# Optimization experiments

Measured on AMD Instinct MI355X. Metric: run time of the kernel, lower is better.

## Reference

```python
import jax, jax.numpy as jnp
import numpy as np

PI = float(np.pi)
N_BINS_POT = 140
TIMESTEP = 0.02
ATOMS = ["N", "CA", "C", "cent"]
ANGLES = [("N", "CA", "C", 0), ("CA", "C", "N", 1), ("C", "N", "CA", 2), ("N", "CA", "cent", 0), ("C", "CA", "cent", 0)]
DIHEDRALS = [("C", "N", "CA", "C", 3), ("N", "CA", "C", "N", 1), ("CA", "C", "N", "CA", 2), ("C", "N", "CA", "cent", 3), ("cent", "CA", "C", "N", 1)]

_gap_ang = (PI - PI / 3) / N_BINS_POT
ANGLE_CENTRES = np.array([PI / 3 + i * _gap_ang + 0.5 * _gap_ang for i in range(N_BINS_POT)][1:-1], dtype=np.float32)  # 138
_gap_dih = 2 * PI / N_BINS_POT
DIH_CENTRES = np.array([-PI + i * _gap_dih - 0.5 * _gap_dih for i in range(N_BINS_POT + 2)][1:-1], dtype=np.float32)  # 140


def safe_norm(v, axis=-1, keepdims=False):
    sq = jnp.sum(v * v, axis=axis, keepdims=keepdims)
    return jnp.where(sq > 0, jnp.sqrt(jnp.where(sq > 0, sq, 1.0)), 0.0)


def normalize(v):
    # torch.nn.functional.normalize with eps=1e-12
    return v / jnp.maximum(safe_norm(v, keepdims=True), 1e-12)


def _gather_force(pots, inds):
    # pots: [n, n_bins]; inds: [b, n] -> 0.5 * (pots[r, i] - pots[r, i+2])
    r = jnp.arange(pots.shape[0])[None, :]
    return 0.5 * (pots[r, inds] - pots[r, inds + 2])


def _accelerations(coords, masses, pair_centres, pair_pots, angle_pots, dih_pots):
    b, n_atoms, _ = coords.shape
    n_res = n_atoms // 4
    # ---- all-pairs distance forces (bin by argmin against per-pair centres, gather) ----
    diffs = coords[:, None, :, :] - coords[:, :, None, :]  # [b, i, j, 3] = c[j] - c[i]
    dists = safe_norm(diffs)  # [b, i, j]
    df = dists.reshape(b, n_atoms * n_atoms)
    inds = jnp.argmin(jnp.abs(pair_centres[None] - df[:, :, None]), axis=2)  # [b, n^2]
    pair_forces = _gather_force(pair_pots, inds).reshape(b, n_atoms, n_atoms)
    norm_diffs = diffs / jnp.maximum(dists, 0.01)[..., None]
    accs = jnp.sum(pair_forces[..., None] * norm_diffs, axis=1) / masses[..., None]
    # ---- bond-angle forces ----
    ac = coords.reshape(b, n_res, 4, 3)
    aa = jnp.zeros_like(ac)
    ang_centres = jnp.asarray(ANGLE_CENTRES)
    for ai, (a1, a2, a3, across) in enumerate(ANGLES):
        i1, i2, i3 = ATOMS.index(a1), ATOMS.index(a2), ATOMS.index(a3)
        if across == 0:
            ba = ac[:, :, i1] - ac[:, :, i2]; bc = ac[:, :, i3] - ac[:, :, i2]; pots = angle_pots[ai]
        elif across == 1:
            ba = ac[:, :-1, i1] - ac[:, :-1, i2]; bc = ac[:, 1:, i3] - ac[:, :-1, i2]; pots = angle_pots[ai][:-1]
        else:
            ba = ac[:, :-1, i1] - ac[:, 1:, i2]; bc = ac[:, 1:, i3] - ac[:, 1:, i2]; pots = angle_pots[ai][1:]
        ban = safe_norm(ba); bcn = safe_norm(bc)
        angs = jnp.arccos(jnp.sum(ba * bc, axis=2) / (ban * bcn))
        ainds = jnp.argmin(jnp.abs(ang_centres[None, None] - angs[:, :, None]), axis=2)
        f = _gather_force(pots, ainds)[..., None]
        cr = jnp.cross(ba, bc)
        fa = f * normalize(jnp.cross(ba, cr)) / ban[..., None]
        fc = f * normalize(jnp.cross(-bc, cr)) / bcn[..., None]
        fb = -fa - fc
        if across == 0:
            aa = aa.at[:, :, i1].add(fa).at[:, :, i2].add(fb).at[:, :, i3].add(fc)
        elif across == 1:
            aa = aa.at[:, :-1, i1].add(fa).at[:, :-1, i2].add(fb).at[:, 1:, i3].add(fc)
        else:
            aa = aa.at[:, :-1, i1].add(fa).at[:, 1:, i2].add(fb).at[:, 1:, i3].add(fc)
    # ---- dihedral forces ----
    dih_centres = jnp.asarray(DIH_CENTRES)
    for di, (a1, a2, a3, a4, across) in enumerate(DIHEDRALS):
        i1, i2, i3, i4 = ATOMS.index(a1), ATOMS.index(a2), ATOMS.index(a3), ATOMS.index(a4)
        if across == 1:
            ab = ac[:, :-1, i2] - ac[:, :-1, i1]; bc = ac[:, :-1, i3] - ac[:, :-1, i2]; cd = ac[:, 1:, i4] - ac[:, :-1, i3]
            pots = dih_pots[di][:-1]
        elif across == 2:
            ab = ac[:, :-1, i2] - ac[:, :-1, i1]; bc = ac[:, 1:, i3] - ac[:, :-1, i2]; cd = ac[:, 1:, i4] - ac[:, 1:, i3]
            pots = dih_pots[di][1:]
        else:  # across == 3
            ab = ac[:, 1:, i2] - ac[:, :-1, i1]; bc = ac[:, 1:, i3] - ac[:, 1:, i2]; cd = ac[:, 1:, i4] - ac[:, 1:, i3]
            pots = dih_pots[di][1:]
        c1 = jnp.cross(ab, bc); c2 = jnp.cross(bc, cd)
        bcn = safe_norm(bc, keepdims=True)
        dihs = jnp.arctan2(jnp.sum(jnp.cross(c1, c2) * bc / bcn, axis=2), jnp.sum(c1 * c2, axis=2))
        dinds = jnp.argmin(jnp.abs(dih_centres[None, None] - dihs[:, :, None]), axis=2)
        f = _gather_force(pots, dinds)[..., None]
        fa = f * normalize(-c1) / safe_norm(ab, keepdims=True)
        fd = f * normalize(c2) / safe_norm(cd, keepdims=True)
        bsq = jnp.squeeze(bcn, -1) ** 2
        t1 = (jnp.sum(ab * bc, axis=2) / bsq)[..., None]
        t2 = (jnp.sum(cd * bc, axis=2) / bsq)[..., None]
        fb = -fa - t1 * fa + t2 * fd  # torque-balancing middle-atom forces
        fc = -fa - fb - fd
        if across == 1:
            aa = aa.at[:, :-1, i1].add(fa).at[:, :-1, i2].add(fb).at[:, :-1, i3].add(fc).at[:, 1:, i4].add(fd)
        elif across == 2:
            aa = aa.at[:, :-1, i1].add(fa).at[:, :-1, i2].add(fb).at[:, 1:, i3].add(fc).at[:, 1:, i4].add(fd)
        else:
            aa = aa.at[:, :-1, i1].add(fa).at[:, 1:, i2].add(fb).at[:, 1:, i3].add(fc).at[:, 1:, i4].add(fd)
    return accs + aa.reshape(b, n_atoms, 3) / masses[..., None]


def _simulate(coords, vels, masses, ff_distances, ff_angles, ff_dihedrals,
              dist_bin_centres, inters_flat, inters_ang, inters_dih, n_steps):
    pair_centres = dist_bin_centres[inters_flat]  # [n^2, 138]
    pair_pots = ff_distances[inters_flat]         # [n^2, 140]
    angle_pots = ff_angles[:, inters_ang]         # [5, n_res, 140]
    dih_pots = ff_dihedrals[:, inters_dih]        # [5, n_res, 142]

    def step(carry, _):
        c, v, a_last = carry
        c = c + v * TIMESTEP + 0.5 * a_last * TIMESTEP * TIMESTEP
        a = _accelerations(c, masses, pair_centres, pair_pots, angle_pots, dih_pots)
        v = v + 0.5 * (a_last + a) * TIMESTEP
        return (c, v, a), None

    (coords, vels, _), _ = jax.lax.scan(step, (coords, vels, jnp.zeros_like(coords)), None, length=n_steps)
    return coords


def setup_inputs() -> dict:
    key = jax.random.key(0)
    ks = jax.random.split(key, 10)
    b, n_res = 1, 100
    n_atoms = n_res * 4
    n2 = n_atoms * n_atoms
    n_dist_types = 4000
    coords = jax.random.normal(ks[0], (b, n_atoms, 3), jnp.float32) * 10.0
    vels = jax.random.normal(ks[1], (b, n_atoms, 3), jnp.float32) * 0.1  # start_temperature = 0.1
    masses = jax.random.uniform(ks[2], (b, n_atoms), jnp.float32, 0.5, 1.5)
    native_coords = jax.random.normal(ks[3], (b, n_atoms, 3), jnp.float32) * 10.0
    ff_distances = jax.random.normal(ks[4], (n_dist_types, 140), jnp.float32) * 0.1
    ff_angles = jax.random.normal(ks[5], (5, 20, 140), jnp.float32) * 0.1
    ff_dihedrals = jax.random.normal(ks[6], (5, 20, 142), jnp.float32) * 0.1
    centres = jnp.linspace(1.0, 15.9, 138, dtype=jnp.float32)
    dist_bin_centres = jnp.tile(centres[None, :], (n_dist_types, 1))
    inters_flat = jax.random.randint(ks[7], (n2,), 0, n_dist_types)
    inters_ang = jax.random.randint(ks[8], (n_res,), 0, 20)
    inters_dih = jax.random.randint(ks[9], (n_res,), 0, 20)
    return {"coords": coords, "vels": vels, "masses": masses, "native_coords": native_coords,
            "ff_distances": ff_distances, "ff_angles": ff_angles, "ff_dihedrals": ff_dihedrals,
            "dist_bin_centres": dist_bin_centres, "inters_flat": inters_flat,
            "inters_ang": inters_ang, "inters_dih": inters_dih, "n_steps": 3}


def reference(coords, vels, masses, native_coords, ff_distances, ff_angles, ff_dihedrals,
              dist_bin_centres, inters_flat, inters_ang, inters_dih, n_steps):
    # native_coords is only used for RMSD reporting in the original; it does not affect the dynamics.
    return _simulate(coords, vels, masses, ff_distances, ff_angles, ff_dihedrals,
                     dist_bin_centres, inters_flat, inters_ang, inters_dih, n_steps)
```

## Files before the change

### kernel.cpp

```cpp
#include <hip/hip_runtime.h>
#include <math.h>

#define N_ATOMS 400
#define N_RES   100
#define DT      0.02f
#define PI_D    3.14159265358979323846
#define NBLK    100
#define NTHR    256

struct V3 { float x, y, z; };
__device__ __forceinline__ V3 v3(float x, float y, float z) { V3 r{x,y,z}; return r; }
__device__ __forceinline__ V3 sub(V3 a, V3 b) { return v3(a.x-b.x, a.y-b.y, a.z-b.z); }
__device__ __forceinline__ V3 neg(V3 a) { return v3(-a.x, -a.y, -a.z); }
__device__ __forceinline__ V3 scale(V3 a, float s) { return v3(a.x*s, a.y*s, a.z*s); }
__device__ __forceinline__ float dot3(V3 a, V3 b) { return a.x*b.x + a.y*b.y + a.z*b.z; }
__device__ __forceinline__ V3 cross3(V3 a, V3 b) {
    return v3(a.y*b.z - a.z*b.y, a.z*b.x - a.x*b.z, a.x*b.y - a.y*b.x);
}
__device__ __forceinline__ float vnorm(V3 a) {
    float s = dot3(a, a);
    return s > 0.0f ? sqrtf(s) : 0.0f;
}
__device__ __forceinline__ V3 normalize3(V3 a) {
    float n = fmaxf(vnorm(a), 1e-12f);
    return scale(a, 1.0f/n);
}

__device__ __forceinline__ int clampi(int i, int lo, int hi) {
    return i < lo ? lo : (i > hi ? hi : i);
}
__device__ __forceinline__ int bin_dist(float d) {
    const float INV = (float)(137.0/14.9);
    return clampi((int)floorf((d - 1.0f)*INV + 0.5f), 0, 137);
}
__device__ __forceinline__ int bin_ang(float a) {
    const float C0  = (float)(PI_D/3.0 + 1.5*((PI_D - PI_D/3.0)/140.0));
    const float INV = (float)(140.0/(PI_D - PI_D/3.0));
    return clampi((int)floorf((a - C0)*INV + 0.5f), 0, 137);
}
__device__ __forceinline__ int bin_dih(float a) {
    const float C0  = (float)(-PI_D + 0.5*(2.0*PI_D/140.0));
    const float INV = (float)(140.0/(2.0*PI_D));
    return clampi((int)floorf((a - C0)*INV + 0.5f), 0, 139);
}

__constant__ int ANG_I[5][3]   = {{0,1,2},{1,2,0},{2,0,1},{0,1,3},{2,1,3}};
__constant__ int ANG_ACROSS[5] = {0,1,2,0,0};
__constant__ int DIH_I[5][4]   = {{2,0,1,2},{0,1,2,0},{1,2,0,1},{2,0,1,3},{3,1,2,0}};
__constant__ int DIH_ACROSS[5] = {3,1,2,3,1};

__device__ __forceinline__ V3 ldpos(const float* c, int res, int atom) {
    int k = (res*4 + atom)*3;
    return v3(c[k], c[k+1], c[k+2]);
}

__device__ __forceinline__ void addOwn(float* sF, int b, int res, int atom, V3 f) {
    if (res == b) {
        atomicAdd(&sF[atom*3+0], f.x);
        atomicAdd(&sF[atom*3+1], f.y);
        atomicAdd(&sF[atom*3+2], f.z);
    }
}

__device__ __forceinline__ void bonded_own(int u, int b, const float* sc,
                              const float* __restrict__ ffa, const float* __restrict__ ffdih,
                              const int* __restrict__ ia, const int* __restrict__ idh,
                              float* sF) {
    int e = u % 10, which = u / 10;
    int r = b - which;
    if (e < 5) {
        int across = ANG_ACROSS[e];
        bool valid = which ? (b >= 1 && across != 0)
                           : (across == 0 || b <= N_RES-2);
        if (!valid) return;
        int i1 = ANG_I[e][0], i2 = ANG_I[e][1], i3 = ANG_I[e][2];
        int o2 = (across == 2) ? 1 : 0;
        int o3 = (across != 0) ? 1 : 0;
        V3 p1 = ldpos(sc, r,     i1);
        V3 p2 = ldpos(sc, r+o2,  i2);
        V3 p3 = ldpos(sc, r+o3,  i3);
        V3 ba = sub(p1, p2);
        V3 bc = sub(p3, p2);
        float ban = vnorm(ba), bcn = vnorm(bc);
        float ca = dot3(ba, bc) / (ban*bcn);
        ca = fminf(1.0f, fmaxf(-1.0f, ca));
        float ang = acosf(ca);
        int ind = bin_ang(ang);
        int potr = (across == 2) ? r+1 : r;
        const float* row = ffa + (e*20 + ia[potr])*140;
        float f = 0.5f*(row[ind] - row[ind+2]);
        V3 cr = cross3(ba, bc);
        V3 fa = scale(normalize3(cross3(ba, cr)), f/ban);
        V3 fc = scale(normalize3(neg(cross3(bc, cr))), f/bcn);
        V3 fb = neg(v3(fa.x+fc.x, fa.y+fc.y, fa.z+fc.z));
        addOwn(sF, b, r,     i1, fa);
        addOwn(sF, b, r+o2,  i2, fb);
        addOwn(sF, b, r+o3,  i3, fc);
    } else {
        int di = e - 5;
        bool valid = which ? (b >= 1) : (b <= N_RES-2);
        if (!valid) return;
        int across = DIH_ACROSS[di];
        int i1 = DIH_I[di][0], i2 = DIH_I[di][1], i3 = DIH_I[di][2], i4 = DIH_I[di][3];
        int o2 = (across == 3) ? 1 : 0;
        int o3 = (across >= 2) ? 1 : 0;
        int o4 = 1;
        V3 p1 = ldpos(sc, r,     i1);
        V3 p2 = ldpos(sc, r+o2,  i2);
        V3 p3 = ldpos(sc, r+o3,  i3);
        V3 p4 = ldpos(sc, r+o4,  i4);
        V3 ab = sub(p2, p1);
        V3 bc = sub(p3, p2);
        V3 cd = sub(p4, p3);
        V3 c1 = cross3(ab, bc);
        V3 c2 = cross3(bc, cd);
        float bcn = vnorm(bc);
        V3 cc = cross3(c1, c2);
        float y = dot3(cc, bc) / bcn;
        float x = dot3(c1, c2);
        float dih = atan2f(y, x);
        int ind = bin_dih(dih);
        int potr = (across == 1) ? r : r+1;
        const float* row = ffdih + (di*20 + idh[potr])*142;
        float f = 0.5f*(row[ind] - row[ind+2]);
        V3 fa = scale(normalize3(neg(c1)), f / vnorm(ab));
        V3 fd = scale(normalize3(c2),      f / vnorm(cd));
        float bsq = bcn*bcn;
        float t1 = dot3(ab, bc)/bsq;
        float t2 = dot3(cd, bc)/bsq;
        V3 fb = v3(-fa.x - t1*fa.x + t2*fd.x,
                   -fa.y - t1*fa.y + t2*fd.y,
                   -fa.z - t1*fa.z + t2*fd.z);
        V3 fc = v3(-fa.x - fb.x - fd.x,
                   -fa.y - fb.y - fd.y,
                   -fa.z - fb.z - fd.z);
        addOwn(sF, b, r,     i1, fa);
        addOwn(sF, b, r+o2,  i2, fb);
        addOwn(sF, b, r+o3,  i3, fc);
        addOwn(sF, b, r+o4,  i4, fd);
    }
}

__device__ __forceinline__ void grid_barrier(int* bar) {
    __syncthreads();
    if (threadIdx.x == 0) {
        __hip_atomic_fetch_add(bar, 1, __ATOMIC_RELEASE, __HIP_MEMORY_SCOPE_AGENT);
        int iters = 0;
        while (__hip_atomic_load(bar, __ATOMIC_RELAXED, __HIP_MEMORY_SCOPE_AGENT) < NBLK) {
            __builtin_amdgcn_s_sleep(1);
            if (++iters > (1 << 24)) break;
        }
        (void)__hip_atomic_load(bar, __ATOMIC_ACQUIRE, __HIP_MEMORY_SCOPE_AGENT);
    }
    __syncthreads();
}

__global__ void init_kernel(const float* __restrict__ cin, const float* __restrict__ vin,
                            float* __restrict__ c, int* __restrict__ bar) {
    int t = blockIdx.x*blockDim.x + threadIdx.x;
    if (t < N_ATOMS*3) c[t] = cin[t] + vin[t]*DT;
    if (t < 4) bar[t] = 0;
}

__global__ void __launch_bounds__(NTHR)
sim_kernel(const float* __restrict__ vin, const float* __restrict__ masses,
           const float* __restrict__ ffd, const float* __restrict__ ffa,
           const float* __restrict__ ffdih, const int* __restrict__ iflat,
           const int* __restrict__ ia, const int* __restrict__ idh,
           float* __restrict__ out, float* __restrict__ c, int* __restrict__ bar)
{
    __shared__ float sc[N_ATOMS*3];
    __shared__ float sF[12];
    const int tid  = threadIdx.x;
    const int b    = blockIdx.x;
    const int lane = tid & 63;
    const int wave = tid >> 6;
    const int j    = b*4 + wave;

    float vv = 0.0f, aa = 0.0f;
    if (tid < 12) vv = vin[b*12 + tid];

    for (int s = 0; s < 2; ++s) {
        for (int t = tid; t < N_ATOMS*3; t += NTHR)
            sc[t] = __hip_atomic_load(&c[t], __ATOMIC_RELAXED, __HIP_MEMORY_SCOPE_AGENT);
        if (tid < 12) sF[tid] = 0.0f;
        __syncthreads();

        if (tid < 20) bonded_own(tid, b, sc, ffa, ffdih, ia, idh, sF);

        float cx = sc[3*j], cy = sc[3*j+1], cz = sc[3*j+2];
        float fx = 0.0f, fy = 0.0f, fz = 0.0f;
        #pragma unroll
        for (int k = 0; k < 7; ++k) {
            int i = lane + 64*k;
            if (k < 6 || i < N_ATOMS) {
                float dx = cx - sc[3*i];
                float dy = cy - sc[3*i+1];
                float dz = cz - sc[3*i+2];
                float d2 = dx*dx + dy*dy + dz*dz;
                float d  = d2 > 0.0f ? sqrtf(d2) : 0.0f;
                int ind  = bin_dist(d);
                int type = iflat[i*N_ATOMS + j];
                const float* row = ffd + type*140;
                float f = 0.5f*(row[ind] - row[ind+2]);
                float w = f / fmaxf(d, 0.01f);
                fx += w*dx; fy += w*dy; fz += w*dz;
            }
        }
        #pragma unroll
        for (int off = 32; off > 0; off >>= 1) {
            fx += __shfl_down(fx, off);
            fy += __shfl_down(fy, off);
            fz += __shfl_down(fz, off);
        }
        if (lane == 0) {
            atomicAdd(&sF[wave*3+0], fx);
            atomicAdd(&sF[wave*3+1], fy);
            atomicAdd(&sF[wave*3+2], fz);
        }
        __syncthreads();

        if (tid < 12) {
            int t = b*12 + tid;
            float a = sF[tid] / masses[b*4 + tid/3];
            vv += 0.5f*(aa + a)*DT;
            aa = a;
            float cc = sc[t] + vv*DT + 0.5f*a*DT*DT;
            if (s == 0)
                __hip_atomic_store(&c[t], cc, __ATOMIC_RELAXED, __HIP_MEMORY_SCOPE_AGENT);
            else
                out[t] = cc;
        }
        if (s == 0) grid_barrier(bar);
    }
}

extern "C" void kernel_launch(void* const* d_in, const int* in_sizes, int n_in,
                              void* d_out, int out_size, void* d_ws, size_t ws_size,
                              hipStream_t stream) {
    const float* coords = (const float*)d_in[0];
    const float* vels   = (const float*)d_in[1];
    const float* masses = (const float*)d_in[2];
    const float* ffd    = (const float*)d_in[4];
    const float* ffa    = (const float*)d_in[5];
    const float* ffdih  = (const float*)d_in[6];
    const int* iflat    = (const int*)d_in[8];
    const int* ia       = (const int*)d_in[9];
    const int* idh      = (const int*)d_in[10];
    float* out = (float*)d_out;

    float* ws  = (float*)d_ws;
    float* c   = ws;
    int*   bar = (int*)(ws + 1200);

    init_kernel<<<5, 256, 0, stream>>>(coords, vels, c, bar);
    sim_kernel<<<NBLK, NTHR, 0, stream>>>(vels, masses, ffd, ffa, ffdih,
                                          iflat, ia, idh, out, c, bar);
}
```

Before: 98.47 us.

## Replace persistent grid barrier with two step kernels and fused init

Swaps the single persistent kernel that used a spin-wait grid barrier for two ordinary launches, one per integration step, with velocity and acceleration handed between them through workspace. The init kernel is removed by having the first kernel compute the drifted coordinates directly into shared memory with float4 loads. Interaction-type indices are now loaded into registers before the coordinate staging, so that latency overlaps with it. This trades the atomic spin barrier for one extra kernel launch boundary, and each kernel reloads the type table.

```diff
diff --git a/kernel.cpp b/kernel.cpp
--- a/kernel.cpp
+++ b/kernel.cpp
@@ -141,33 +141,52 @@
     }
 }
 
-__device__ __forceinline__ void grid_barrier(int* bar) {
-    __syncthreads();
-    if (threadIdx.x == 0) {
-        __hip_atomic_fetch_add(bar, 1, __ATOMIC_RELEASE, __HIP_MEMORY_SCOPE_AGENT);
-        int iters = 0;
-        while (__hip_atomic_load(bar, __ATOMIC_RELAXED, __HIP_MEMORY_SCOPE_AGENT) < NBLK) {
-            __builtin_amdgcn_s_sleep(1);
-            if (++iters > (1 << 24)) break;
+__device__ __forceinline__ void force_phase(int b, int tid, int lane, int wave,
+                              const float* sc, float* sF, const int* ty,
+                              const float* __restrict__ ffd, const float* __restrict__ ffa,
+                              const float* __restrict__ ffdih, const int* __restrict__ ia,
+                              const int* __restrict__ idh) {
+    if (tid < 20) bonded_own(tid, b, sc, ffa, ffdih, ia, idh, sF);
+
+    int j = b*4 + wave;
+    float cx = sc[3*j], cy = sc[3*j+1], cz = sc[3*j+2];
+    float fx = 0.0f, fy = 0.0f, fz = 0.0f;
+    #pragma unroll
+    for (int k = 0; k < 7; ++k) {
+        int i = lane + 64*k;
+        if (k < 6 || i < N_ATOMS) {
+            float dx = cx - sc[3*i];
+            float dy = cy - sc[3*i+1];
+            float dz = cz - sc[3*i+2];
+            float d2 = dx*dx + dy*dy + dz*dz;
+            float d  = d2 > 0.0f ? sqrtf(d2) : 0.0f;
+            int ind  = bin_dist(d);
+            const float* row = ffd + ty[k]*140;
+            float f = 0.5f*(row[ind] - row[ind+2]);
+            float w = f / fmaxf(d, 0.01f);
+            fx += w*dx; fy += w*dy; fz += w*dz;
         }
-        (void)__hip_atomic_load(bar, __ATOMIC_ACQUIRE, __HIP_MEMORY_SCOPE_AGENT);
-    }
-    __syncthreads();
-}
-
-__global__ void init_kernel(const float* __restrict__ cin, const float* __restrict__ vin,
-                            float* __restrict__ c, int* __restrict__ bar) {
-    int t = blockIdx.x*blockDim.x + threadIdx.x;
-    if (t < N_ATOMS*3) c[t] = cin[t] + vin[t]*DT;
-    if (t < 4) bar[t] = 0;
+    }
+    #pragma unroll
+    for (int off = 32; off > 0; off >>= 1) {
+        fx += __shfl_down(fx, off);
+        fy += __shfl_down(fy, off);
+        fz += __shfl_down(fz, off);
+    }
+    if (lane == 0) {
+        atomicAdd(&sF[wave*3+0], fx);
+        atomicAdd(&sF[wave*3+1], fy);
+        atomicAdd(&sF[wave*3+2], fz);
+    }
 }
 
 __global__ void __launch_bounds__(NTHR)
-sim_kernel(const float* __restrict__ vin, const float* __restrict__ masses,
-           const float* __restrict__ ffd, const float* __restrict__ ffa,
-           const float* __restrict__ ffdih, const int* __restrict__ iflat,
-           const int* __restrict__ ia, const int* __restrict__ idh,
-           float* __restrict__ out, float* __restrict__ c, int* __restrict__ bar)
+stepA(const float* __restrict__ cin, const float* __restrict__ vin,
+      const float* __restrict__ masses, const float* __restrict__ ffd,
+      const float* __restrict__ ffa, const float* __restrict__ ffdih,
+      const int* __restrict__ iflat, const int* __restrict__ ia,
+      const int* __restrict__ idh, float* __restrict__ c2,
+      float* __restrict__ v1, float* __restrict__ a1)
 {
     __shared__ float sc[N_ATOMS*3];
     __shared__ float sF[12];
@@ -177,61 +196,72 @@
     const int wave = tid >> 6;
     const int j    = b*4 + wave;
 
-    float vv = 0.0f, aa = 0.0f;
-    if (tid < 12) vv = vin[b*12 + tid];
-
-    for (int s = 0; s < 2; ++s) {
-        for (int t = tid; t < N_ATOMS*3; t += NTHR)
-            sc[t] = __hip_atomic_load(&c[t], __ATOMIC_RELAXED, __HIP_MEMORY_SCOPE_AGENT);
-        if (tid < 12) sF[tid] = 0.0f;
-        __syncthreads();
-
-        if (tid < 20) bonded_own(tid, b, sc, ffa, ffdih, ia, idh, sF);
-
-        float cx = sc[3*j], cy = sc[3*j+1], cz = sc[3*j+2];
-        float fx = 0.0f, fy = 0.0f, fz = 0.0f;
-        #pragma unroll
-        for (int k = 0; k < 7; ++k) {
-            int i = lane + 64*k;
-            if (k < 6 || i < N_ATOMS) {
-                float dx = cx - sc[3*i];
-                float dy = cy - sc[3*i+1];
-                float dz = cz - sc[3*i+2];
-                float d2 = dx*dx + dy*dy + dz*dz;
-                float d  = d2 > 0.0f ? sqrtf(d2) : 0.0f;
-                int ind  = bin_dist(d);
-                int type = iflat[i*N_ATOMS + j];
-                const float* row = ffd + type*140;
-                float f = 0.5f*(row[ind] - row[ind+2]);
-                float w = f / fmaxf(d, 0.01f);
-                fx += w*dx; fy += w*dy; fz += w*dz;
-            }
-        }
-        #pragma unroll
-        for (int off = 32; off > 0; off >>= 1) {
-            fx += __shfl_down(fx, off);
-            fy += __shfl_down(fy, off);
-            fz += __shfl_down(fz, off);
-        }
-        if (lane == 0) {
-            atomicAdd(&sF[wave*3+0], fx);
-            atomicAdd(&sF[wave*3+1], fy);
-            atomicAdd(&sF[wave*3+2], fz);
-        }
-        __syncthreads();
-
-        if (tid < 12) {
-            int t = b*12 + tid;
-            float a = sF[tid] / masses[b*4 + tid/3];
-            vv += 0.5f*(aa + a)*DT;
-            aa = a;
-            float cc = sc[t] + vv*DT + 0.5f*a*DT*DT;
-            if (s == 0)
-                __hip_atomic_store(&c[t], cc, __ATOMIC_RELAXED, __HIP_MEMORY_SCOPE_AGENT);
-            else
-                out[t] = cc;
-        }
-        if (s == 0) grid_barrier(bar);
+    int ty[7];
+    #pragma unroll
+    for (int k = 0; k < 7; ++k) {
+        int i = lane + 64*k;
+        ty[k] = (k < 6 || i < N_ATOMS) ? iflat[i*N_ATOMS + j] : 0;
+    }
+
+    for (int q = tid; q < 300; q += NTHR) {
+        float4 cv = ((const float4*)cin)[q];
+        float4 vv = ((const float4*)vin)[q];
+        float4 r;
+        r.x = cv.x + vv.x*DT; r.y = cv.y + vv.y*DT;
+        r.z = cv.z + vv.z*DT; r.w = cv.w + vv.w*DT;
+        ((float4*)sc)[q] = r;
+    }
+    if (tid < 12) sF[tid] = 0.0f;
+    __syncthreads();
+
+    force_phase(b, tid, lane, wave, sc, sF, ty, ffd, ffa, ffdih, ia, idh);
+    __syncthreads();
+
+    if (tid < 12) {
+        int t = b*12 + tid;
+        float a = sF[tid] / masses[b*4 + tid/3];
+        float v = vin[t] + 0.5f*a*DT;
+        float cc = sc[t] + v*DT + 0.5f*a*DT*DT;
+        c2[t] = cc; v1[t] = v; a1[t] = a;
+    }
+}
+
+__global__ void __launch_bounds__(NTHR)
+stepB(const float* __restrict__ masses, const float* __restrict__ ffd,
+      const float* __restrict__ ffa, const float* __restrict__ ffdih,
+      const int* __restrict__ iflat, const int* __restrict__ ia,
+      const int* __restrict__ idh, const float* __restrict__ c2,
+      const float* __restrict__ v1, const float* __restrict__ a1,
+      float* __restrict__ out)
+{
+    __shared__ float sc[N_ATOMS*3];
+    __shared__ float sF[12];
+    const int tid  = threadIdx.x;
+    const int b    = blockIdx.x;
+    const int lane = tid & 63;
+    const int wave = tid >> 6;
+    const int j    = b*4 + wave;
+
+    int ty[7];
+    #pragma unroll
+    for (int k = 0; k < 7; ++k) {
+        int i = lane + 64*k;
+        ty[k] = (k < 6 || i < N_ATOMS) ? iflat[i*N_ATOMS + j] : 0;
+    }
+
+    for (int q = tid; q < 300; q += NTHR)
+        ((float4*)sc)[q] = ((const float4*)c2)[q];
+    if (tid < 12) sF[tid] = 0.0f;
+    __syncthreads();
+
+    force_phase(b, tid, lane, wave, sc, sF, ty, ffd, ffa, ffdih, ia, idh);
+    __syncthreads();
+
+    if (tid < 12) {
+        int t = b*12 + tid;
+        float a = sF[tid] / masses[b*4 + tid/3];
+        float v = v1[t] + 0.5f*(a1[t] + a)*DT;
+        out[t] = sc[t] + v*DT + 0.5f*a*DT*DT;
     }
 }
 
@@ -249,11 +279,13 @@
     const int* idh      = (const int*)d_in[10];
     float* out = (float*)d_out;
 
-    float* ws  = (float*)d_ws;
-    float* c   = ws;
-    int*   bar = (int*)(ws + 1200);
-
-    init_kernel<<<5, 256, 0, stream>>>(coords, vels, c, bar);
-    sim_kernel<<<NBLK, NTHR, 0, stream>>>(vels, masses, ffd, ffa, ffdih,
-                                          iflat, ia, idh, out, c, bar);
-}
+    float* ws = (float*)d_ws;
+    float* c2 = ws;
+    float* v1 = ws + 1200;
+    float* a1 = ws + 2400;
+
+    stepA<<<NBLK, NTHR, 0, stream>>>(coords, vels, masses, ffd, ffa, ffdih,
+                                     iflat, ia, idh, c2, v1, a1);
+    stepB<<<NBLK, NTHR, 0, stream>>>(masses, ffd, ffa, ffdih,
+                                     iflat, ia, idh, c2, v1, a1, out);
+}
```

After: 92.71 us. 5.9% less time.
